# Performance work log

Measured on AMD Instinct MI355X. Metric: run time of the kernel, lower is better.

Reference implementation:

```python
import jax, jax.numpy as jnp
import numpy as np
import math

L = 2          # num_layers
H = 1024       # hidden_dim
NH = 16        # num_heads
HD = H // NH   # head_dim = 64
M = 4096       # mlp_dim
GRIDS = [(2, 32, 32), (1, 32, 32)]  # (t,h,w) per image -> 2048 + 1024 = 3072 tokens
THETA = 10000.0
EPS = 1e-5


def _rope_cos_sin(grids, head_dim):
    # Rope2DPosEmbRepeated: interleaved (x,y) complex rotations, repeated over t.
    n = head_dim // 4
    freqs = 1.0 / (THETA ** (np.arange(0, head_dim, 4, dtype=np.float64)[:n] / head_dim))
    parts = []
    for t, h, w in grids:
        ys, xs = np.meshgrid(np.arange(h), np.arange(w), indexing='ij')
        xa = xs.reshape(-1, 1).astype(np.float64) * freqs  # [h*w, n]
        ya = ys.reshape(-1, 1).astype(np.float64) * freqs
        ang = np.stack([xa, ya], axis=-1).reshape(-1, head_dim // 2)  # interleave x,y
        parts.append(np.tile(ang, (t, 1)))
    ang = np.concatenate(parts, axis=0).astype(np.float32)  # [S, head_dim//2]
    return jnp.asarray(np.cos(ang)), jnp.asarray(np.sin(ang))


def _segment_ids(grids):
    lens = [t * h * w for t, h, w in grids]
    return jnp.asarray(np.repeat(np.arange(len(lens)), lens))


def _layernorm(x, g, b):
    mu = jnp.mean(x, axis=-1, keepdims=True)
    var = jnp.mean(jnp.square(x - mu), axis=-1, keepdims=True)
    return (x - mu) * jax.lax.rsqrt(var + EPS) * g + b


def _apply_rope(x, cos, sin):
    # x: [S, NH, HD]; cos/sin: [S, HD//2] -> broadcast over heads (unsqueeze(-2))
    xr = x.reshape(x.shape[0], x.shape[1], HD // 2, 2)
    a, b = xr[..., 0], xr[..., 1]
    c = cos[:, None, :]
    s = sin[:, None, :]
    oa = a * c - b * s
    ob = a * s + b * c
    return jnp.stack([oa, ob], axis=-1).reshape(x.shape)


def setup_inputs() -> dict:
    key = jax.random.key(0)
    ks = jax.random.split(key, 8)
    S = sum(t * h * w for t, h, w in GRIDS)
    sH = 1.0 / math.sqrt(H)
    sM = 1.0 / math.sqrt(M)
    return {
        'hidden_states': jax.random.normal(ks[0], (S, H), jnp.float32),
        'grid_thws': jnp.asarray(np.array(GRIDS, dtype=np.int32)),
        'ln0_g': jnp.ones((L, H), jnp.float32),
        'ln0_b': jnp.zeros((L, H), jnp.float32),
        'wqkv': jax.random.normal(ks[1], (L, 3 * H, H), jnp.float32) * sH,
        'wo': jax.random.normal(ks[2], (L, H, H), jnp.float32) * sH,
        'ln1_g': jnp.ones((L, H), jnp.float32),
        'ln1_b': jnp.zeros((L, H), jnp.float32),
        'fc0_w': jax.random.normal(ks[3], (L, M, H), jnp.float32) * math.sqrt(2.0 / H),
        'fc0_b': jnp.zeros((L, M), jnp.float32),
        'fc1_w': jax.random.normal(ks[4], (L, H, M), jnp.float32) * math.sqrt(2.0 / M),
        'fc1_b': jnp.zeros((L, H), jnp.float32),
        'fln_g': jnp.ones((H,), jnp.float32),
        'fln_b': jnp.zeros((H,), jnp.float32),
    }


def reference(hidden_states, grid_thws, ln0_g, ln0_b, wqkv, wo, ln1_g, ln1_b,
              fc0_w, fc0_b, fc1_w, fc1_b, fln_g, fln_b):
    grids = [tuple(int(v) for v in row) for row in np.asarray(grid_thws)]
    S = hidden_states.shape[0]
    cos, sin = _rope_cos_sin(grids, HD)
    seg = _segment_ids(grids)
    mask = seg[:, None] == seg[None, :]  # block-diagonal [S, S]
    scale = 1.0 / math.sqrt(HD)

    x = hidden_states
    for i in range(L):
        h = _layernorm(x, ln0_g[i], ln0_b[i])
        qkv = (h @ wqkv[i].T).reshape(S, 3, NH, HD)
        q, k, v = qkv[:, 0], qkv[:, 1], qkv[:, 2]
        q = _apply_rope(q, cos, sin)
        k = _apply_rope(k, cos, sin)
        scores = jnp.einsum('qhd,khd->hqk', q, k) * scale
        scores = jnp.where(mask[None], scores, -1e30)
        attn = jax.nn.softmax(scores, axis=-1)
        o = jnp.einsum('hqk,khd->qhd', attn, v).reshape(S, H)
        x = x + o @ wo[i].T
        h2 = _layernorm(x, ln1_g[i], ln1_b[i])
        mlp = jax.nn.gelu(h2 @ fc0_w[i].T + fc0_b[i], approximate=False) @ fc1_w[i].T + fc1_b[i]
        x = x + mlp
    return _layernorm(x, fln_g, fln_b)
```

## Files before the change

### kernel.cpp

```cpp
#include <hip/hip_runtime.h>
#include <hip/hip_bf16.h>
#include <cstdint>
#include <math.h>

constexpr int ST   = 3072;
constexpr int HH   = 1024;
constexpr int NHD  = 16;
constexpr int DH   = 64;
constexpr int MMLP = 4096;
constexpr int SEG0 = 2048;

using short8 = __attribute__((ext_vector_type(8))) short;
using f32x4  = __attribute__((ext_vector_type(4))) float;

#if __has_builtin(__builtin_amdgcn_exp2f)
#define EXP2F __builtin_amdgcn_exp2f
#else
#define EXP2F exp2f
#endif

#if __has_builtin(__builtin_amdgcn_rcpf)
#define RCPF __builtin_amdgcn_rcpf
#else
#define RCPF(x) (1.f / (x))
#endif

__device__ __forceinline__ unsigned short f2bf(float f) {
  unsigned int u = __float_as_uint(f);
  u += 0x7fffu + ((u >> 16) & 1u);
  return (unsigned short)(u >> 16);
}

__device__ __forceinline__ unsigned int pkbf(float lo, float hi) {
  union { __bf16 h[2]; unsigned int u; } r;
  r.h[0] = (__bf16)lo;
  r.h[1] = (__bf16)hi;
  return r.u;
}

__device__ __forceinline__ float bf2f_lo(unsigned int u) {
  return __uint_as_float(u << 16);
}
__device__ __forceinline__ float bf2f_hi(unsigned int u) {
  return __uint_as_float(u & 0xffff0000u);
}

__device__ __forceinline__ void g2l16(const void* g, void* l) {
  __builtin_amdgcn_global_load_lds(
      (const __attribute__((address_space(1))) unsigned int*)g,
      (__attribute__((address_space(3))) unsigned int*)l, 16, 0, 0);
}

__device__ __forceinline__ float erf_fast(float z) {
  const float az = fabsf(z);
  const float t1 = RCPF(1.f + 0.3275911f * az);
  const float poly =
      t1 * (0.254829592f +
            t1 * (-0.284496736f +
                  t1 * (1.421413741f +
                        t1 * (-1.453152027f + t1 * 1.061405429f))));
  const float e = EXP2F(-az * az * 1.4426950408889634f);
  const float v = 1.f - poly * e;
  return (z < 0.f) ? -v : v;
}

__global__ void cast_all(const float* __restrict__ s0,
                         const float* __restrict__ s1,
                         const float* __restrict__ s2,
                         const float* __restrict__ s3,
                         ushort4* __restrict__ dst) {
  const int i = blockIdx.x * blockDim.x + threadIdx.x;
  const float4* src;
  int off;
  if (i < 1572864)      { src = (const float4*)s0; off = i; }
  else if (i < 2097152) { src = (const float4*)s1; off = i - 1572864; }
  else if (i < 4194304) { src = (const float4*)s2; off = i - 2097152; }
  else                  { src = (const float4*)s3; off = i - 4194304; }
  const float4 v = src[off];
  ushort4 u;
  u.x = f2bf(v.x); u.y = f2bf(v.y); u.z = f2bf(v.z); u.w = f2bf(v.w);
  dst[i] = u;
}

__global__ void ln_kernel(const float* __restrict__ x,
                          const float* __restrict__ g,
                          const float* __restrict__ b,
                          unsigned short* obf) {
  const int s = blockIdx.x;
  const int t = threadIdx.x;
  const float4 v = ((const float4*)(x + (size_t)s * HH))[t];
  float s1 = v.x + v.y + v.z + v.w;
  float s2 = v.x * v.x + v.y * v.y + v.z * v.z + v.w * v.w;
#pragma unroll
  for (int off = 32; off > 0; off >>= 1) {
    s1 += __shfl_down(s1, off);
    s2 += __shfl_down(s2, off);
  }
  __shared__ float red[8];
  __shared__ float stat[2];
  const int wv = t >> 6, ln = t & 63;
  if (ln == 0) { red[wv] = s1; red[4 + wv] = s2; }
  __syncthreads();
  if (t == 0) {
    float a1 = red[0] + red[1] + red[2] + red[3];
    float a2 = red[4] + red[5] + red[6] + red[7];
    float mu = a1 * (1.f / HH);
    float var = a2 * (1.f / HH) - mu * mu;
    stat[0] = mu;
    stat[1] = rsqrtf(var + 1e-5f);
  }
  __syncthreads();
  const float mu = stat[0], rs = stat[1];
  const float4 gg = ((const float4*)g)[t];
  const float4 bb = ((const float4*)b)[t];
  ushort4 u;
  u.x = f2bf((v.x - mu) * rs * gg.x + bb.x);
  u.y = f2bf((v.y - mu) * rs * gg.y + bb.y);
  u.z = f2bf((v.z - mu) * rs * gg.z + bb.z);
  u.w = f2bf((v.w - mu) * rs * gg.w + bb.w);
  ((ushort4*)(obf + (size_t)s * HH))[t] = u;
}

template <int NS>
__global__ void ln_comb(const float* __restrict__ xin,
                        const unsigned short* __restrict__ Pb,
                        const float* __restrict__ bias,
                        const float* __restrict__ g,
                        const float* __restrict__ b,
                        float* __restrict__ xout,
                        unsigned short* obf, float* of) {
  const int s = blockIdx.x;
  const int t = threadIdx.x;
  const size_t row = (size_t)s * HH;
  const size_t sl = (size_t)ST * HH;
  float4 v = ((const float4*)(xin + row))[t];
#pragma unroll
  for (int c = 0; c < NS; ++c) {
    const uint2 p = ((const uint2*)(Pb + c * sl + row))[t];
    v.x += bf2f_lo(p.x); v.y += bf2f_hi(p.x);
    v.z += bf2f_lo(p.y); v.w += bf2f_hi(p.y);
  }
  if (bias) {
    const float4 bb4 = ((const float4*)bias)[t];
    v.x += bb4.x; v.y += bb4.y; v.z += bb4.z; v.w += bb4.w;
  }
  if (xout) ((float4*)(xout + row))[t] = v;
  float s1 = v.x + v.y + v.z + v.w;
  float s2 = v.x * v.x + v.y * v.y + v.z * v.z + v.w * v.w;
#pragma unroll
  for (int off = 32; off > 0; off >>= 1) {
    s1 += __shfl_down(s1, off);
    s2 += __shfl_down(s2, off);
  }
  __shared__ float red[8];
  __shared__ float stat[2];
  const int wv = t >> 6, ln = t & 63;
  if (ln == 0) { red[wv] = s1; red[4 + wv] = s2; }
  __syncthreads();
  if (t == 0) {
    float a1 = red[0] + red[1] + red[2] + red[3];
    float a2 = red[4] + red[5] + red[6] + red[7];
    float mu = a1 * (1.f / HH);
    float var = a2 * (1.f / HH) - mu * mu;
    stat[0] = mu;
    stat[1] = rsqrtf(var + 1e-5f);
  }
  __syncthreads();
  const float mu = stat[0], rs = stat[1];
  const float4 gg = ((const float4*)g)[t];
  const float4 bb = ((const float4*)b)[t];
  float4 o;
  o.x = (v.x - mu) * rs * gg.x + bb.x;
  o.y = (v.y - mu) * rs * gg.y + bb.y;
  o.z = (v.z - mu) * rs * gg.z + bb.z;
  o.w = (v.w - mu) * rs * gg.w + bb.w;
  if (obf) {
    ushort4 u;
    u.x = f2bf(o.x); u.y = f2bf(o.y); u.z = f2bf(o.z); u.w = f2bf(o.w);
    ((ushort4*)(obf + row))[t] = u;
  } else {
    ((float4*)(of + row))[t] = o;
  }
}

__global__ void rope_tables(float2* __restrict__ cs2) {
  const int s = blockIdx.x;
  const int j = threadIdx.x;
  const int p = (s < SEG0) ? (s & 1023) : (s - SEG0);
  const int pos = (j & 1) ? (p >> 5) : (p & 31);
  const int f = j >> 1;
  const double freq = pow(10000.0, -(double)f / 16.0);
  const double ang = (double)pos * freq;
  cs2[s * 32 + j] = make_float2((float)cos(ang), (float)sin(ang));
}

template <int MODE>
__launch_bounds__(256)
__global__ void gemm_bt(const unsigned short* __restrict__ A,
                        const unsigned short* __restrict__ B,
                        float* Cf, unsigned short* Cb,
                        const float* __restrict__ bias,
                        int N, int K) {
  __shared__ unsigned short Sl[16384];
  unsigned short* Al = Sl;
  unsigned short* Bl = Sl + 8192;
  const int tid = threadIdx.x;
  const int lane = tid & 63;
  const int wave = tid >> 6;
  const int col = lane & 15;
  const int quad = lane >> 4;
  const int m0 = blockIdx.y * 128;
  const int n0 = blockIdx.x * 128;
  const int wm = (wave & 1) * 64;
  const int wn = (wave >> 1) * 64;

  int kFrom = 0, kTo = K;
  if (MODE == 4) {
    const int kc = K / gridDim.z;
    kFrom = blockIdx.z * kc;
    kTo = kFrom + kc;
  }

  f32x4 acc[4][4] = {};

  const int tr = tid >> 3;
  const int pb = tid & 7;
  const int kb = pb ^ (tr & 7);
  const unsigned short* Ag = A + (size_t)(m0 + tr) * K + kb * 8;
  const unsigned short* Bg = B + (size_t)(n0 + tr) * K + kb * 8;
  unsigned short* Alw = Al + (size_t)tid * 8;
  unsigned short* Blw = Bl + (size_t)tid * 8;

#pragma unroll
  for (int it = 0; it < 4; ++it) {
    g2l16(Ag + (size_t)(it * 32) * K + kFrom, Alw + it * 2048);
    g2l16(Bg + (size_t)(it * 32) * K + kFrom, Blw + it * 2048);
  }
  __syncthreads();

  for (int k0 = kFrom; k0 < kTo; k0 += 64) {
    short8 af[4][2], bfr[4][2];
#pragma unroll
    for (int kk = 0; kk < 2; ++kk) {
#pragma unroll
      for (int mt = 0; mt < 4; ++mt) {
        int r = wm + mt * 16 + col;
        int kp = (kk * 4 + quad) ^ (r & 7);
        af[mt][kk] = *(const short8*)(Al + r * 64 + kp * 8);
      }
#pragma unroll
      for (int nt = 0; nt < 4; ++nt) {
        int r = wn + nt * 16 + col;
        int kp = (kk * 4 + quad) ^ (r & 7);
        bfr[nt][kk] = *(const short8*)(Bl + r * 64 + kp * 8);
      }
    }
    __syncthreads();
    const int kn = k0 + 64;
    if (kn < kTo) {
#pragma unroll
      for (int it = 0; it < 4; ++it) {
        g2l16(Ag + (size_t)(it * 32) * K + kn, Alw + it * 2048);
        g2l16(Bg + (size_t)(it * 32) * K + kn, Blw + it * 2048);
      }
    }
    __builtin_amdgcn_sched_barrier(0);
#pragma unroll
    for (int kk = 0; kk < 2; ++kk)
#pragma unroll
      for (int mt = 0; mt < 4; ++mt)
#pragma unroll
        for (int nt = 0; nt < 4; ++nt)
          acc[mt][nt] = __builtin_amdgcn_mfma_f32_16x16x32_bf16(
              af[mt][kk], bfr[nt][kk], acc[mt][nt], 0, 0, 0);
    __syncthreads();
  }

  if (MODE == 5) {
    const int bufsel = n0 >> 10;
    if (bufsel == 2) {
      unsigned int* T32 = (unsigned int*)Sl;
#pragma unroll
      for (int mt = 0; mt < 4; ++mt) {
        const int d0 = (wm + mt * 16 + quad * 4) >> 1;
#pragma unroll
        for (int nt = 0; nt < 4; ++nt) {
          const int cl = wn + nt * 16 + col;
          const int swz = (cl & 7) << 3;
          uint2 w;
          w.x = (unsigned)f2bf(acc[mt][nt][0]) |
                ((unsigned)f2bf(acc[mt][nt][1]) << 16);
          w.y = (unsigned)f2bf(acc[mt][nt][2]) |
                ((unsigned)f2bf(acc[mt][nt][3]) << 16);
          *(uint2*)&T32[cl * 64 + (d0 ^ swz)] = w;
        }
      }
      __syncthreads();
      unsigned short* vt = (unsigned short*)Cf;
      const int cl = tid >> 1;
      const int half = tid & 1;
      const int swz = (cl & 7) << 3;
      const int gch = (n0 & 1023) + cl;
      unsigned short* dst = vt + (size_t)gch * ST + m0 + half * 64;
#pragma unroll
      for (int j4 = 0; j4 < 8; ++j4) {
        const int d = half * 32 + j4 * 4;
        const uint4 v4 = *(const uint4*)&T32[cl * 64 + (d ^ swz)];
        *(uint4*)(dst + j4 * 8) = v4;
      }
    } else {
      const float2* tab = (const float2*)bias;
      unsigned short* out = Cb + (size_t)bufsel * (ST * HH);
      const float SQ = 0.125f * 1.4426950408889634f;
#pragma unroll
      for (int mt = 0; mt < 4; ++mt) {
#pragma unroll
        for (int r = 0; r < 4; ++r) {
          const int gr = m0 + wm + mt * 16 + quad * 4 + r;
#pragma unroll
          for (int nt = 0; nt < 4; ++nt) {
            const int gc = n0 + wn + nt * 16 + col;
            const int c1023 = gc & 1023;
            const int j = (c1023 & 63) >> 1;
            const float2 cs = tab[gr * 32 + j];
            const float v = acc[mt][nt][r];
            const float vp = __shfl_xor(v, 1);
            float res = (lane & 1) ? (vp * cs.y + v * cs.x)
                                   : (v * cs.x - vp * cs.y);
            if (bufsel == 0) res *= SQ;
            const float rp = __shfl_xor(res, 1);
            if (!(lane & 1))
              *(unsigned int*)(out + (size_t)gr * HH + c1023) =
                  (unsigned)f2bf(res) | ((unsigned)f2bf(rp) << 16);
          }
        }
      }
    }
    return;
  }
  const size_t zoff = (MODE == 4) ? (size_t)blockIdx.z * ST * N : 0;
#pragma unroll
  for (int mt = 0; mt < 4; ++mt) {
#pragma unroll
    for (int r = 0; r < 4; ++r) {
      const int gr = m0 + wm + mt * 16 + quad * 4 + r;
#pragma unroll
      for (int nt = 0; nt < 4; ++nt) {
        const int gc = n0 + wn + nt * 16 + col;
        float res = acc[mt][nt][r];
        if (MODE == 2) {
          const float tt = res + bias[gc];
          res = 0.5f * tt * (1.f + erf_fast(tt * 0.70710678f));
        }
        const float rp = __shfl_xor(res, 1);
        if (!(lane & 1))
          *(unsigned int*)(Cb + zoff + (size_t)gr * N + gc) =
              (unsigned)f2bf(res) | ((unsigned)f2bf(rp) << 16);
      }
    }
  }
}

__launch_bounds__(256)
__global__ void attn_flash(const unsigned short* __restrict__ Qb,
                           const unsigned short* __restrict__ Kb,
                           const unsigned short* __restrict__ VT,
                           float* __restrict__ Op01,
                           float* __restrict__ Op23,
                           float* __restrict__ lbuf) {
  const int gid = blockIdx.x + 80 * blockIdx.y;
  const int xcd = gid & 7;
  const int slot = gid >> 3;
  const int g = xcd * 10 + (slot >> 4);
  const int member = slot & 15;
  const int h = g / 5;
  const int cg = g % 5;
  int qt, chunk, s0;
  if (cg < 4) { qt = member; chunk = cg; s0 = 0; }
  else { qt = 16 + (member & 7); chunk = member >> 3; s0 = SEG0; }
  const int q0 = qt * 128;
  const int koff = s0 + chunk * 512;

  const int tid = threadIdx.x;
  const int lane = tid & 63;
  const int wave = tid >> 6;
  const int col = lane & 15;
  const int quad = lane >> 4;

  __shared__ unsigned short Sl[16384];
  unsigned short* Kl = Sl;
  unsigned short* Vl = Sl + 8192;
  unsigned int* Plb = (unsigned int*)Sl;

  short8 qf[2][2];
#pragma unroll
  for (int mt = 0; mt < 2; ++mt) {
    const unsigned short* qrow =
        Qb + (size_t)(q0 + wave * 32 + mt * 16 + col) * HH + h * DH;
    qf[mt][0] = *(const short8*)(qrow + quad * 8);
    qf[mt][1] = *(const short8*)(qrow + 32 + quad * 8);
  }

  short8 ones;
#pragma unroll
  for (int j = 0; j < 8; ++j) ones[j] = (short)0x3F80;

  f32x4 accO[2][4] = {};
  f32x4 accL[2] = {};
  const float SHIFT = 16.f;

  const int trK = tid >> 3, pbK = tid & 7;
  const int kbK = pbK ^ (trK & 7);
  const int trV = tid >> 4, pbV = tid & 15;
  const int prow = ((wave * 2) * 16 + col) * 20;

  for (int kb0 = 0; kb0 < 512; kb0 += 128) {
#pragma unroll
    for (int it = 0; it < 4; ++it)
      g2l16(Kb + (size_t)(koff + kb0 + it * 32 + trK) * HH + h * DH + kbK * 8,
            (unsigned short*)Kl + it * 2048 + (size_t)tid * 8);
#pragma unroll
    for (int it = 0; it < 4; ++it) {
      const int d = it * 16 + trV;
      const int kbv = pbV ^ (d & 7);
      g2l16(VT + (size_t)(h * 64 + d) * ST + koff + kb0 + kbv * 8,
            (unsigned short*)Vl + it * 2048 + (size_t)tid * 8);
    }
    __syncthreads();

    f32x4 sc[2][8];
#pragma unroll
    for (int nt = 0; nt < 8; ++nt) {
      const int r = nt * 16 + col;
      const short8 kf0 = *(const short8*)(Kl + r * 64 + ((quad) ^ (r & 7)) * 8);
      const short8 kf1 = *(const short8*)(Kl + r * 64 + ((4 + quad) ^ (r & 7)) * 8);
#pragma unroll
      for (int mt = 0; mt < 2; ++mt) {
        f32x4 z = {};
        z = __builtin_amdgcn_mfma_f32_16x16x32_bf16(kf0, qf[mt][0], z, 0, 0, 0);
        sc[mt][nt] = __builtin_amdgcn_mfma_f32_16x16x32_bf16(kf1, qf[mt][1], z, 0, 0, 0);
      }
    }
    __syncthreads();

#pragma unroll
    for (int kd = 0; kd < 4; ++kd) {
#pragma unroll
      for (int mt = 0; mt < 2; ++mt) {
#pragma unroll
        for (int ntl = 0; ntl < 2; ++ntl) {
          const f32x4 s4 = sc[mt][kd * 2 + ntl];
          uint2 w;
          w.x = pkbf(EXP2F(s4[0] - SHIFT), EXP2F(s4[1] - SHIFT));
          w.y = pkbf(EXP2F(s4[2] - SHIFT), EXP2F(s4[3] - SHIFT));
          *(uint2*)&Plb[prow + mt * 320 + ntl * 8 + quad * 2] = w;
        }
      }
      short8 pf[2];
#pragma unroll
      for (int mt = 0; mt < 2; ++mt)
        pf[mt] = *(const short8*)&Plb[prow + mt * 320 + quad * 4];
#pragma unroll
      for (int mt = 0; mt < 2; ++mt)
        accL[mt] = __builtin_amdgcn_mfma_f32_16x16x32_bf16(pf[mt], ones,
                                                           accL[mt], 0, 0, 0);
#pragma unroll
      for (int dt = 0; dt < 4; ++dt) {
        const int rv = dt * 16 + col;
        const int pbv2 = (kd * 4 + quad) ^ (rv & 7);
        const short8 vf = *(const short8*)(Vl + rv * 128 + pbv2 * 8);
#pragma unroll
        for (int mt = 0; mt < 2; ++mt)
          accO[mt][dt] = __builtin_amdgcn_mfma_f32_16x16x32_bf16(
              pf[mt], vf, accO[mt][dt], 0, 0, 0);
      }
    }
    __syncthreads();
  }

  float* Opc = (chunk < 2) ? (Op01 + (size_t)chunk * (ST * HH))
                           : (Op23 + (size_t)(chunk - 2) * (ST * HH));
#pragma unroll
  for (int mt = 0; mt < 2; ++mt)
#pragma unroll
    for (int r = 0; r < 4; ++r) {
      const int row = q0 + wave * 32 + mt * 16 + quad * 4 + r;
#pragma unroll
      for (int dt = 0; dt < 4; ++dt)
        Opc[(size_t)row * HH + h * DH + dt * 16 + col] = accO[mt][dt][r];
      if (col == 0)
        lbuf[((size_t)chunk * ST + row) * NHD + h] = accL[mt][r];
    }
}

__global__ void attn_combine(const float* __restrict__ Op01,
                             const float* __restrict__ Op23,
                             const float* __restrict__ lbuf,
                             unsigned short* __restrict__ out) {
  const int s = blockIdx.x;
  const int t = threadIdx.x;
  const int h = t >> 4;
  const int d0 = (t & 15) * 4;
  const int nc = (s < SEG0) ? 4 : 2;
  float L = 0.f;
  float4 o = make_float4(0.f, 0.f, 0.f, 0.f);
  for (int c = 0; c < nc; ++c) {
    const float* Opc = (c < 2) ? (Op01 + (size_t)c * (ST * HH))
                               : (Op23 + (size_t)(c - 2) * (ST * HH));
    L += lbuf[((size_t)c * ST + s) * NHD + h];
    const float4 v = *(const float4*)(Opc + (size_t)s * HH + h * DH + d0);
    o.x += v.x; o.y += v.y; o.z += v.z; o.w += v.w;
  }
  const float inv = 1.f / L;
  ushort4 u;
  u.x = f2bf(o.x * inv); u.y = f2bf(o.y * inv);
  u.z = f2bf(o.z * inv); u.w = f2bf(o.w * inv);
  ((ushort4*)(out + (size_t)s * HH))[t] = u;
}

extern "C" void kernel_launch(void* const* d_in, const int* in_sizes, int n_in,
                              void* d_out, int out_size, void* d_ws, size_t ws_size,
                              hipStream_t stream) {
  const float* hs   = (const float*)d_in[0];
  const float* ln0g = (const float*)d_in[2];
  const float* ln0b = (const float*)d_in[3];
  const float* wqkv = (const float*)d_in[4];
  const float* wo   = (const float*)d_in[5];
  const float* ln1g = (const float*)d_in[6];
  const float* ln1b = (const float*)d_in[7];
  const float* fc0w = (const float*)d_in[8];
  const float* fc0b = (const float*)d_in[9];
  const float* fc1w = (const float*)d_in[10];
  const float* fc1b = (const float*)d_in[11];
  const float* fln_g = (const float*)d_in[12];
  const float* fln_b = (const float*)d_in[13];

  char* ws = (char*)d_ws;
  unsigned short* wqkv_bf = (unsigned short*)(ws + 0);
  unsigned short* wo_bf   = (unsigned short*)(ws + 12582912);
  unsigned short* fc0_bf  = (unsigned short*)(ws + 16777216);
  unsigned short* fc1_bf  = (unsigned short*)(ws + 33554432);
  float*          x       = (float*)(ws + 50331648);
  unsigned short* abf     = (unsigned short*)(ws + 62914560);
  unsigned short* gelu_bf = (unsigned short*)(ws + 69206016);
  unsigned short* Qbf     = (unsigned short*)(ws + 132120576);
  unsigned short* Kbf     = (unsigned short*)(ws + 138412032);
  float*          cs2tab  = (float*)(ws + 150994944);
  unsigned short* VT    = (unsigned short*)(ws + 94371840);
  float*          Op    = (float*)(ws + 100663296);
  float*          Op23  = (float*)(ws + 69206016);
  float*          lbuf  = (float*)(ws + 144703488);
  unsigned short* Pbuf  = (unsigned short*)(ws + 94371840);

  cast_all<<<24576, 256, 0, stream>>>(wqkv, wo, fc0w, fc1w, (ushort4*)ws);
  rope_tables<<<ST, 32, 0, stream>>>((float2*)cs2tab);

  for (int i = 0; i < 2; ++i) {
    if (i == 0)
      ln_kernel<<<ST, 256, 0, stream>>>(hs, ln0g, ln0b, abf);
    gemm_bt<5><<<dim3(24, 24), 256, 0, stream>>>(
        abf, wqkv_bf + (size_t)i * 3 * HH * HH, (float*)VT, Qbf, cs2tab,
        3 * HH, HH);
    attn_flash<<<dim3(80, 16), 256, 0, stream>>>(Qbf, Kbf, VT, Op, Op23, lbuf);
    attn_combine<<<ST, 256, 0, stream>>>(Op, Op23, lbuf, abf);
    gemm_bt<4><<<dim3(8, 24, 4), 256, 0, stream>>>(
        abf, wo_bf + (size_t)i * HH * HH, nullptr, Pbuf, nullptr, HH, HH);
    ln_comb<4><<<ST, 256, 0, stream>>>(
        (i == 0) ? hs : x, Pbuf, nullptr, ln1g + i * HH, ln1b + i * HH,
        x, abf, nullptr);
    gemm_bt<2><<<dim3(32, 24), 256, 0, stream>>>(
        abf, fc0_bf + (size_t)i * MMLP * HH, nullptr, gelu_bf, fc0b + i * MMLP,
        MMLP, HH);
    gemm_bt<4><<<dim3(8, 24, 4), 256, 0, stream>>>(
        gelu_bf, fc1_bf + (size_t)i * HH * MMLP, nullptr, Pbuf, nullptr,
        HH, MMLP);
    if (i == 0)
      ln_comb<4><<<ST, 256, 0, stream>>>(x, Pbuf, fc1b, ln0g + HH, ln0b + HH,
                                         x, abf, nullptr);
    else
      ln_comb<4><<<ST, 256, 0, stream>>>(x, Pbuf, fc1b + HH, fln_g, fln_b,
                                         nullptr, nullptr, (float*)d_out);
  }
}
```

Baseline: 557.9 us.

## Double-buffer GEMM shared-memory tiles with K-step of 32

The GEMM main loop changes from a single LDS buffer with a 64-wide K step to two LDS buffers with a 32-wide K step. The next tile's global-to-LDS load is issued into the alternate buffer before the current tile's fragment reads and MFMAs, and one of the two barriers per iteration is removed. The XOR swizzle is rewritten for 32-element rows. The intent is to overlap global loads with compute and cut synchronisation. In exchange there are twice as many iterations, each with less MFMA work to hide load latency, and a new bank-conflict pattern.

```diff
diff --git a/kernel.cpp b/kernel.cpp
--- a/kernel.cpp
+++ b/kernel.cpp
@@ -202,8 +202,6 @@
                         const float* __restrict__ bias,
                         int N, int K) {
   __shared__ unsigned short Sl[16384];
-  unsigned short* Al = Sl;
-  unsigned short* Bl = Sl + 8192;
   const int tid = threadIdx.x;
   const int lane = tid & 63;
   const int wave = tid >> 6;
@@ -223,57 +221,51 @@
 
   f32x4 acc[4][4] = {};
 
-  const int tr = tid >> 3;
-  const int pb = tid & 7;
-  const int kb = pb ^ (tr & 7);
-  const unsigned short* Ag = A + (size_t)(m0 + tr) * K + kb * 8;
-  const unsigned short* Bg = B + (size_t)(n0 + tr) * K + kb * 8;
-  unsigned short* Alw = Al + (size_t)tid * 8;
-  unsigned short* Blw = Bl + (size_t)tid * 8;
-
-#pragma unroll
-  for (int it = 0; it < 4; ++it) {
-    g2l16(Ag + (size_t)(it * 32) * K + kFrom, Alw + it * 2048);
-    g2l16(Bg + (size_t)(it * 32) * K + kFrom, Blw + it * 2048);
+  const int trS = tid >> 2;
+  const int pbS = tid & 3;
+  const int kbS = pbS ^ ((trS >> 2) & 3);
+  const unsigned short* Ag = A + (size_t)(m0 + trS) * K + kbS * 8;
+  const unsigned short* Bg = B + (size_t)(n0 + trS) * K + kbS * 8;
+  const int cR = quad ^ (col >> 2);
+
+#pragma unroll
+  for (int it = 0; it < 2; ++it) {
+    g2l16(Ag + (size_t)(it * 64) * K + kFrom, Sl + it * 2048 + (size_t)tid * 8);
+    g2l16(Bg + (size_t)(it * 64) * K + kFrom,
+          Sl + 4096 + it * 2048 + (size_t)tid * 8);
   }
   __syncthreads();
 
-  for (int k0 = kFrom; k0 < kTo; k0 += 64) {
-    short8 af[4][2], bfr[4][2];
-#pragma unroll
-    for (int kk = 0; kk < 2; ++kk) {
-#pragma unroll
-      for (int mt = 0; mt < 4; ++mt) {
-        int r = wm + mt * 16 + col;
-        int kp = (kk * 4 + quad) ^ (r & 7);
-        af[mt][kk] = *(const short8*)(Al + r * 64 + kp * 8);
-      }
-#pragma unroll
-      for (int nt = 0; nt < 4; ++nt) {
-        int r = wn + nt * 16 + col;
-        int kp = (kk * 4 + quad) ^ (r & 7);
-        bfr[nt][kk] = *(const short8*)(Bl + r * 64 + kp * 8);
-      }
-    }
+  int ct = 0;
+  for (int k0 = kFrom; k0 < kTo; k0 += 32) {
+    const int kn = k0 + 32;
+    if (kn < kTo) {
+      unsigned short* nb = Sl + (ct ^ 1) * 8192;
+#pragma unroll
+      for (int it = 0; it < 2; ++it) {
+        g2l16(Ag + (size_t)(it * 64) * K + kn, nb + it * 2048 + (size_t)tid * 8);
+        g2l16(Bg + (size_t)(it * 64) * K + kn,
+              nb + 4096 + it * 2048 + (size_t)tid * 8);
+      }
+    }
+    __builtin_amdgcn_sched_barrier(0);
+    const unsigned short* Ab = Sl + ct * 8192;
+    const unsigned short* Bb = Ab + 4096;
+    short8 af[4], bfr[4];
+#pragma unroll
+    for (int mt = 0; mt < 4; ++mt)
+      af[mt] = *(const short8*)(Ab + (wm + mt * 16 + col) * 32 + cR * 8);
+#pragma unroll
+    for (int nt = 0; nt < 4; ++nt)
+      bfr[nt] = *(const short8*)(Bb + (wn + nt * 16 + col) * 32 + cR * 8);
+#pragma unroll
+    for (int mt = 0; mt < 4; ++mt)
+#pragma unroll
+      for (int nt = 0; nt < 4; ++nt)
+        acc[mt][nt] = __builtin_amdgcn_mfma_f32_16x16x32_bf16(
+            af[mt], bfr[nt], acc[mt][nt], 0, 0, 0);
     __syncthreads();
-    const int kn = k0 + 64;
-    if (kn < kTo) {
-#pragma unroll
-      for (int it = 0; it < 4; ++it) {
-        g2l16(Ag + (size_t)(it * 32) * K + kn, Alw + it * 2048);
-        g2l16(Bg + (size_t)(it * 32) * K + kn, Blw + it * 2048);
-      }
-    }
-    __builtin_amdgcn_sched_barrier(0);
-#pragma unroll
-    for (int kk = 0; kk < 2; ++kk)
-#pragma unroll
-      for (int mt = 0; mt < 4; ++mt)
-#pragma unroll
-        for (int nt = 0; nt < 4; ++nt)
-          acc[mt][nt] = __builtin_amdgcn_mfma_f32_16x16x32_bf16(
-              af[mt][kk], bfr[nt][kk], acc[mt][nt], 0, 0, 0);
-    __syncthreads();
+    ct ^= 1;
   }
 
   if (MODE == 5) {
```

Result: slower. 586.6 us (+5.1%).
